# Kernel tuning notes

Hardware: AMD Instinct MI355X
Metric: run time of the kernel (lower is better)

The kernel has to match this reference:

```python
import jax, jax.numpy as jnp
import numpy as np

B, S, D, H, DK, DL, DR = 2, 2048, 2048, 16, 128, 512, 64
EPS = 1e-6


def _rmsnorm(x, w):
    # torch nn.RMSNorm: x / sqrt(mean(x^2) + eps) * weight, over last dim
    return x * jax.lax.rsqrt(jnp.mean(x * x, axis=-1, keepdims=True) + EPS) * w


def _rope_tables(seq_len, d):
    # matches RoPE.__init__: half of the d//2 freqs are real, half are zero
    quarter = d // 4
    freq = (1.0 / 10000.0) ** jnp.linspace(0.0, 1.0, quarter, dtype=jnp.float32)
    freq = jnp.concatenate([freq, jnp.zeros((quarter,), jnp.float32)])
    theta = jnp.arange(seq_len, dtype=jnp.float32)[:, None] * freq[None, :]  # (S, d//2)
    return jnp.cos(theta), jnp.sin(theta)


def _apply_rope(x, cos, sin):
    # x: (B, H, S, d); cos/sin: (S, d//2)
    half = x.shape[-1] // 2
    x1, x2 = x[..., :half], x[..., half:]
    c = cos[None, None, :, :]
    s = sin[None, None, :, :]
    y1 = x1 * c + x2 * s
    y2 = -x1 * s + x2 * c
    return jnp.concatenate([y1, y2], axis=-1)


def setup_inputs() -> dict:
    key = jax.random.key(0)
    ks = jax.random.split(key, 9)
    w = lambda k, sh: jax.random.normal(k, sh, jnp.float32) * 0.02
    return {
        "x": jax.random.normal(ks[0], (B, S, D), jnp.float32),
        "wq": w(ks[1], (D, H * DK)),
        "w_kv_down": w(ks[2], (D, DL)),
        "w_k_rope": w(ks[3], (DL, H * DR)),
        "w_k_nope": w(ks[4], (DL, H * (DK - DR))),
        "wv": w(ks[5], (DL, H * DK)),
        "wo": w(ks[6], (H * DK, D)),
        "q_norm_w": jnp.ones((DK,), jnp.float32),
        "k_norm_w": jnp.ones((DK,), jnp.float32),
    }


def reference(x, wq, w_kv_down, w_k_rope, w_k_nope, wv, wo, q_norm_w, k_norm_w):
    b, s, _ = x.shape
    # Q path
    q = (x @ wq).reshape(b, s, H, DK)
    q = _rmsnorm(q, q_norm_w).transpose(0, 2, 1, 3)  # (B,H,S,DK)
    # low-rank KV latent
    latent = x @ w_kv_down  # (B,S,DL)
    v = (latent @ wv).reshape(b, s, H, DK).transpose(0, 2, 1, 3)
    k_rope = (latent @ w_k_rope).reshape(b, s, H, DR).transpose(0, 2, 1, 3)
    k_nope = (latent @ w_k_nope).reshape(b, s, H, DK - DR).transpose(0, 2, 1, 3)
    # decoupled RoPE on first DR dims of q and on k_rope
    cos, sin = _rope_tables(s, DR)
    q = jnp.concatenate([_apply_rope(q[..., :DR], cos, sin), q[..., DR:]], axis=-1)
    k = jnp.concatenate([_apply_rope(k_rope, cos, sin), k_nope], axis=-1)
    k = _rmsnorm(k, k_norm_w)
    # causal SDPA, scale 1/sqrt(DK)
    scale = 1.0 / np.sqrt(DK).astype(np.float32)
    scores = jnp.einsum('bhqd,bhkd->bhqk', q, k) * scale
    causal = jnp.tril(jnp.ones((s, s), bool))
    scores = jnp.where(causal[None, None], scores, jnp.finfo(scores.dtype).min)
    attn = jax.nn.softmax(scores, axis=-1)
    out = jnp.einsum('bhqk,bhkd->bhqd', attn, v)
    out = out.transpose(0, 2, 1, 3).reshape(b, s, H * DK)
    return out @ wo
```

## Files before the change

### kernel.cpp

```cpp
#include <hip/hip_runtime.h>
#include <hip/hip_bf16.h>
#include <math.h>

#define B_ 2
#define S_ 2048
#define D_ 2048
#define H_ 16
#define DK_ 128
#define DL_ 512
#define DR_ 64
#define BS_ (B_ * S_)

typedef __attribute__((ext_vector_type(8))) short short8;
typedef __attribute__((ext_vector_type(4))) float f32x4;

static __device__ __forceinline__ ushort f2b(float f) {
    union { __hip_bfloat16 h; ushort u; } cvt;
    cvt.h = __float2bfloat16(f);
    return cvt.u;
}
static __device__ __forceinline__ float b2f(ushort u) {
    return __uint_as_float(((uint)u) << 16);
}

#define GLOAD_LDS16(g, l)                                                         \
    __builtin_amdgcn_global_load_lds(                                             \
        (const __attribute__((address_space(1))) void*)(g),                       \
        (__attribute__((address_space(3))) void*)(l), 16, 0, 0)

__global__ __launch_bounds__(256) void cvt_f32_bf16(const float* __restrict__ in,
                                                    ushort* __restrict__ out, int n) {
    int i = (blockIdx.x * 256 + threadIdx.x) * 4;
    if (i >= n) return;
    float4 v = *(const float4*)(in + i);
    ushort4 o;
    o.x = f2b(v.x); o.y = f2b(v.y); o.z = f2b(v.z); o.w = f2b(v.w);
    *(ushort4*)(out + i) = o;
}

__global__ __launch_bounds__(256) void transpose_cvt(const float* __restrict__ in,
                                                     ushort* __restrict__ out,
                                                     int R, int C) {
    __shared__ float tile[32][33];
    int c0 = blockIdx.x * 32, r0 = blockIdx.y * 32;
    int tx = threadIdx.x, ty = threadIdx.y;
#pragma unroll
    for (int i = 0; i < 4; ++i)
        tile[ty + i * 8][tx] = in[(size_t)(r0 + ty + i * 8) * C + c0 + tx];
    __syncthreads();
#pragma unroll
    for (int i = 0; i < 4; ++i)
        out[(size_t)(c0 + ty + i * 8) * R + r0 + tx] = f2b(tile[tx][ty + i * 8]);
}

__global__ __launch_bounds__(256) void v_transpose(const ushort* __restrict__ krnv,
                                                   ushort* __restrict__ vt) {
    __shared__ ushort tile[32][34];
    const int bh = blockIdx.z, b = bh >> 4, h = bh & 15;
    const int d0 = blockIdx.x * 32, s0 = blockIdx.y * 32;
    const int tx = threadIdx.x, ty = threadIdx.y;
    const ushort* src = krnv + (size_t)(b * 2048 + s0) * 4096 + 2048 + h * 128 + d0;
#pragma unroll
    for (int i = 0; i < 4; ++i)
        tile[ty + i * 8][tx] = src[(size_t)(ty + i * 8) * 4096 + tx];
    __syncthreads();
    ushort* dst = vt + ((size_t)bh * 128 + d0) * 2048 + s0;
#pragma unroll
    for (int i = 0; i < 4; ++i)
        dst[(size_t)(ty + i * 8) * 2048 + tx] = tile[tx][ty + i * 8];
}

__global__ __launch_bounds__(256) void rope_tables(float* __restrict__ cosT,
                                                   float* __restrict__ sinT) {
    int idx = blockIdx.x * 256 + threadIdx.x;
    int s = idx >> 5, j = idx & 31;
    float c = 1.f, sn = 0.f;
    if (j < 16) {
        float t = (float)j * (1.0f / 15.0f);
        float f = powf(10000.0f, -t);
        float th = (float)s * f;
        c = cosf(th);
        sn = sinf(th);
    }
    cosT[idx] = c;
    sinT[idx] = sn;
}

template <int OUT_BF16>
__global__ __launch_bounds__(256) void gemm_bt(const ushort* __restrict__ A,
                                               const ushort* __restrict__ BT,
                                               void* __restrict__ Cv,
                                               int M, int N, int K) {
    __shared__ __align__(16) ushort As[128 * 32];
    __shared__ __align__(16) ushort Bs[128 * 32];
    const int tid = threadIdx.x;
    const int lane = tid & 63, wave = tid >> 6;
    const int wr = wave >> 1, wc = wave & 1;
    const int row0 = blockIdx.y * 128, col0 = blockIdx.x * 128;
    const int fr = lane & 15, kg = (lane >> 4) * 8;

    f32x4 acc[4][4] = {};

    const int sr = tid >> 2;
    const int sc8 = (tid & 3) * 8;
    const ushort* ga = A + (size_t)(row0 + sr) * K + sc8;
    const ushort* gb = BT + (size_t)(col0 + sr) * K + sc8;
    ushort* asDst = As + (size_t)(wave * 64) * 8;
    ushort* bsDst = Bs + (size_t)(wave * 64) * 8;

    for (int k0 = 0; k0 < K; k0 += 32) {
        GLOAD_LDS16(ga + k0, asDst);
        GLOAD_LDS16(ga + (size_t)64 * K + k0, asDst + 256 * 8);
        GLOAD_LDS16(gb + k0, bsDst);
        GLOAD_LDS16(gb + (size_t)64 * K + k0, bsDst + 256 * 8);
        __syncthreads();

        short8 af[4], bfr[4];
#pragma unroll
        for (int m = 0; m < 4; ++m)
            af[m] = *(const short8*)&As[(wr * 64 + m * 16 + fr) * 32 + kg];
#pragma unroll
        for (int n = 0; n < 4; ++n)
            bfr[n] = *(const short8*)&Bs[(wc * 64 + n * 16 + fr) * 32 + kg];
#pragma unroll
        for (int m = 0; m < 4; ++m)
#pragma unroll
            for (int n = 0; n < 4; ++n)
                acc[m][n] = __builtin_amdgcn_mfma_f32_16x16x32_bf16(af[m], bfr[n],
                                                                    acc[m][n], 0, 0, 0);
        __syncthreads();
    }

    const int rbase = row0 + wr * 64 + (lane >> 4) * 4;
    const int cbase = col0 + wc * 64 + fr;
    if constexpr (OUT_BF16) {
        ushort* C = (ushort*)Cv;
#pragma unroll
        for (int m = 0; m < 4; ++m)
#pragma unroll
            for (int n = 0; n < 4; ++n)
#pragma unroll
                for (int j = 0; j < 4; ++j)
                    C[(size_t)(rbase + m * 16 + j) * N + cbase + n * 16] = f2b(acc[m][n][j]);
    } else {
        float* C = (float*)Cv;
#pragma unroll
        for (int m = 0; m < 4; ++m)
#pragma unroll
            for (int n = 0; n < 4; ++n)
#pragma unroll
                for (int j = 0; j < 4; ++j)
                    C[(size_t)(rbase + m * 16 + j) * N + cbase + n * 16] = acc[m][n][j];
    }
}

__global__ __launch_bounds__(256) void q_norm_rope(const ushort* __restrict__ qp,
                                                   const float* __restrict__ w,
                                                   const float* __restrict__ cosT,
                                                   const float* __restrict__ sinT,
                                                   ushort* __restrict__ qb) {
    const int lane = threadIdx.x & 63, wave = threadIdx.x >> 6;
    const int rowId = blockIdx.x * 4 + wave;
    const int bs = rowId >> 4, h = rowId & 15;
    const int s = bs & (S_ - 1);
    const float scale = 0.08838834764831845f;
    const ushort* src = qp + (size_t)bs * 2048 + h * 128;
    float e0 = b2f(src[lane]), e1 = b2f(src[64 + lane]);
    float ss = e0 * e0 + e1 * e1;
#pragma unroll
    for (int m = 1; m < 64; m <<= 1) ss += __shfl_xor(ss, m, 64);
    float r = rsqrtf(ss * (1.0f / 128.0f) + 1e-6f);
    float xn0 = e0 * r * w[lane];
    float xn1 = e1 * r * w[64 + lane];
    int j = lane & 31;
    float c = cosT[s * 32 + j], sn = sinT[s * 32 + j];
    float p = __shfl_xor(xn0, 32, 64);
    float y0 = (lane < 32) ? (xn0 * c + p * sn) : (-p * sn + xn0 * c);
    ushort* dst = qb + (size_t)bs * 2048 + h * 128;
    dst[lane] = f2b(y0 * scale);
    dst[64 + lane] = f2b(xn1 * scale);
}

__global__ __launch_bounds__(256) void k_assemble(const ushort* __restrict__ krnv,
                                                  const float* __restrict__ w,
                                                  const float* __restrict__ cosT,
                                                  const float* __restrict__ sinT,
                                                  ushort* __restrict__ kb) {
    const int lane = threadIdx.x & 63, wave = threadIdx.x >> 6;
    const int rowId = blockIdx.x * 4 + wave;
    const int bs = rowId >> 4, h = rowId & 15;
    const int s = bs & (S_ - 1);
    float e0 = b2f(krnv[(size_t)bs * 4096 + h * 64 + lane]);
    float e1 = b2f(krnv[(size_t)bs * 4096 + 1024 + h * 64 + lane]);
    int j = lane & 31;
    float c = cosT[s * 32 + j], sn = sinT[s * 32 + j];
    float p = __shfl_xor(e0, 32, 64);
    float y0 = (lane < 32) ? (e0 * c + p * sn) : (-p * sn + e0 * c);
    float ss = y0 * y0 + e1 * e1;
#pragma unroll
    for (int m = 1; m < 64; m <<= 1) ss += __shfl_xor(ss, m, 64);
    float r = rsqrtf(ss * (1.0f / 128.0f) + 1e-6f);
    ushort* dst = kb + (size_t)bs * 2048 + h * 128;
    dst[lane] = f2b(y0 * r * w[lane]);
    dst[64 + lane] = f2b(e1 * r * w[64 + lane]);
}

__global__ __launch_bounds__(512) void attn_fwd(const ushort* __restrict__ Q,
                                                const ushort* __restrict__ Kb,
                                                const ushort* __restrict__ Vt,
                                                ushort* __restrict__ Ob) {
    __shared__ __align__(16) ushort Kls[2][8192];
    __shared__ __align__(16) ushort Vls[2][8192];
    __shared__ __align__(16) ushort Pls[8][1024];
    const int tid = threadIdx.x, lane = tid & 63, wave = tid >> 6;
    const int bh = (int)blockIdx.x * 4 + ((int)blockIdx.y & 3);
    const int qp = (int)blockIdx.y >> 2;
    const int b = bh >> 4, h = bh & 15;
    const int fr = lane & 15, g = lane >> 4;
    const int sfr = lane >> 2, sg = lane & 3;

    const ushort* qbase = Q + (size_t)(b * S_) * 2048 + h * 128;
    const ushort* kbase = Kb + (size_t)(b * S_) * 2048 + h * 128;
    const ushort* vtbase = Vt + (size_t)bh * 128 * 2048;
    ushort* myP = Pls[wave];

    auto stage = [&](int kt0, int bufi) {
#pragma unroll
        for (int i = 0; i < 2; ++i) {
            const int si = wave * 2 + i;
            GLOAD_LDS16(kbase + (size_t)(kt0 + (si >> 2) * 16 + sfr) * 2048 +
                            (si & 3) * 32 + sg * 8,
                        &Kls[bufi][si * 512]);
            GLOAD_LDS16(vtbase + (size_t)((si >> 1) * 16 + sfr) * 2048 + kt0 +
                            (si & 1) * 32 + sg * 8,
                        &Vls[bufi][si * 512]);
        }
    };

#pragma unroll 1
    for (int pi = 0; pi < 2; ++pi) {
        const int qi = pi ? qp : 15 - qp;
        const int q0 = qi * 128;
        const int nt = 2 * qi + 2;

        short8 qf[4];
        const ushort* qrow = qbase + (size_t)(q0 + wave * 16 + fr) * 2048;
#pragma unroll
        for (int kb = 0; kb < 4; ++kb) qf[kb] = *(const short8*)(qrow + kb * 32 + g * 8);

        f32x4 Oacc[8] = {};
        float mrow[4], lrow[4];
#pragma unroll
        for (int j = 0; j < 4; ++j) { mrow[j] = -1e30f; lrow[j] = 0.f; }

        stage(0, 0);
        for (int t = 0; t < nt; ++t) {
            __syncthreads();
            if (t + 1 < nt) stage((t + 1) * 64, (t + 1) & 1);
            const ushort* Kc = Kls[t & 1];
            const ushort* Vc = Vls[t & 1];
            const int kt0 = t * 64;
            f32x4 sc[4] = {};
            __builtin_amdgcn_s_setprio(1);
#pragma unroll
            for (int n = 0; n < 4; ++n)
#pragma unroll
                for (int kb = 0; kb < 4; ++kb) {
                    short8 kf = *(const short8*)&Kc[(n * 4 + kb) * 512 + fr * 32 + g * 8];
                    sc[n] = __builtin_amdgcn_mfma_f32_16x16x32_bf16(qf[kb], kf, sc[n], 0, 0, 0);
                }
            __builtin_amdgcn_s_setprio(0);
            if (t >= nt - 2) {
#pragma unroll
                for (int n = 0; n < 4; ++n) {
                    int kpos = kt0 + n * 16 + fr;
#pragma unroll
                    for (int j = 0; j < 4; ++j) {
                        int qr = q0 + wave * 16 + g * 4 + j;
                        if (kpos > qr) sc[n][j] = -1e30f;
                    }
                }
            }
            float tmax[4];
#pragma unroll
            for (int j = 0; j < 4; ++j)
                tmax[j] = fmaxf(fmaxf(sc[0][j], sc[1][j]), fmaxf(sc[2][j], sc[3][j]));
#pragma unroll
            for (int m = 1; m < 16; m <<= 1)
#pragma unroll
                for (int j = 0; j < 4; ++j) tmax[j] = fmaxf(tmax[j], __shfl_xor(tmax[j], m, 64));
            float dm = fmaxf(fmaxf(tmax[0] - mrow[0], tmax[1] - mrow[1]),
                             fmaxf(tmax[2] - mrow[2], tmax[3] - mrow[3]));
            if (!__all(dm <= 8.0f)) {
                float alpha[4];
#pragma unroll
                for (int j = 0; j < 4; ++j) {
                    float mn = fmaxf(mrow[j], tmax[j]);
                    alpha[j] = __expf(mrow[j] - mn);
                    mrow[j] = mn;
                    lrow[j] *= alpha[j];
                }
#pragma unroll
                for (int n8 = 0; n8 < 8; ++n8)
#pragma unroll
                    for (int j = 0; j < 4; ++j) Oacc[n8][j] *= alpha[j];
            }
            float rsum[4] = {0.f, 0.f, 0.f, 0.f};
#pragma unroll
            for (int n = 0; n < 4; ++n)
#pragma unroll
                for (int j = 0; j < 4; ++j) {
                    float pv = __expf(sc[n][j] - mrow[j]);
                    sc[n][j] = pv;
                    rsum[j] += pv;
                }
#pragma unroll
            for (int m = 1; m < 16; m <<= 1)
#pragma unroll
                for (int j = 0; j < 4; ++j) rsum[j] += __shfl_xor(rsum[j], m, 64);
#pragma unroll
            for (int j = 0; j < 4; ++j) lrow[j] += rsum[j];
#pragma unroll
            for (int n = 0; n < 4; ++n)
#pragma unroll
                for (int j = 0; j < 4; ++j) {
                    int q = g * 4 + j;
                    int cg = n * 2 + (fr >> 3);
                    int cs = (((cg ^ (q >> 1)) & 7) << 3) | (fr & 7);
                    myP[q * 64 + cs] = f2b(sc[n][j]);
                }
            short8 pa[2];
#pragma unroll
            for (int ks = 0; ks < 2; ++ks) {
                int pg = ((ks * 4 + g) ^ (fr >> 1)) & 7;
                pa[ks] = *(const short8*)&myP[fr * 64 + (pg << 3)];
            }
            __builtin_amdgcn_s_setprio(1);
#pragma unroll
            for (int n8 = 0; n8 < 8; ++n8)
#pragma unroll
                for (int ks = 0; ks < 2; ++ks) {
                    short8 vf = *(const short8*)&Vc[(n8 * 2 + ks) * 512 + fr * 32 + g * 8];
                    Oacc[n8] = __builtin_amdgcn_mfma_f32_16x16x32_bf16(pa[ks], vf, Oacc[n8], 0, 0, 0);
                }
            __builtin_amdgcn_s_setprio(0);
        }
#pragma unroll
        for (int j = 0; j < 4; ++j) {
            int qr = q0 + wave * 16 + g * 4 + j;
            float inv = 1.0f / lrow[j];
            ushort* orow = Ob + (size_t)(b * S_ + qr) * 2048 + h * 128;
#pragma unroll
            for (int n8 = 0; n8 < 8; ++n8) orow[n8 * 16 + fr] = f2b(Oacc[n8][j] * inv);
        }
        __syncthreads();
    }
}

extern "C" void kernel_launch(void* const* d_in, const int* in_sizes, int n_in,
                              void* d_out, int out_size, void* d_ws, size_t ws_size,
                              hipStream_t stream) {
    (void)in_sizes; (void)n_in; (void)out_size; (void)ws_size;
    const float* x = (const float*)d_in[0];
    const float* wq = (const float*)d_in[1];
    const float* w_kv_down = (const float*)d_in[2];
    const float* w_k_rope = (const float*)d_in[3];
    const float* w_k_nope = (const float*)d_in[4];
    const float* wv = (const float*)d_in[5];
    const float* wo = (const float*)d_in[6];
    const float* q_norm_w = (const float*)d_in[7];
    const float* k_norm_w = (const float*)d_in[8];
    float* out = (float*)d_out;

    char* ws = (char*)d_ws;
    size_t off = 0;
    auto alloc = [&](size_t bytes) {
        off = (off + 255) & ~(size_t)255;
        void* p = ws + off;
        off += bytes;
        return p;
    };
    ushort* xb = (ushort*)alloc((size_t)BS_ * 2048 * 2);
    ushort* wq_t = (ushort*)alloc((size_t)2048 * 2048 * 2);
    ushort* wkv_t = (ushort*)alloc((size_t)512 * 2048 * 2);
    ushort* wkrnv_t = (ushort*)alloc((size_t)4096 * 512 * 2);
    ushort* wo_t = (ushort*)alloc((size_t)2048 * 2048 * 2);
    ushort* q_pre_b = (ushort*)alloc((size_t)BS_ * 2048 * 2);
    ushort* latent_b = (ushort*)alloc((size_t)BS_ * 512 * 2);
    ushort* krnv_b = (ushort*)alloc((size_t)BS_ * 4096 * 2);
    ushort* q_b = (ushort*)alloc((size_t)BS_ * 2048 * 2);
    ushort* k_b = (ushort*)alloc((size_t)BS_ * 2048 * 2);
    ushort* vt = (ushort*)alloc((size_t)BS_ * 2048 * 2);
    ushort* ao_b = (ushort*)alloc((size_t)BS_ * 2048 * 2);
    float* cosT = (float*)alloc((size_t)S_ * 32 * 4);
    float* sinT = (float*)alloc((size_t)S_ * 32 * 4);

    cvt_f32_bf16<<<(BS_ * 2048 / 4 + 255) / 256, 256, 0, stream>>>(x, xb, BS_ * 2048);
    transpose_cvt<<<dim3(2048 / 32, 2048 / 32), dim3(32, 8), 0, stream>>>(wq, wq_t, 2048, 2048);
    transpose_cvt<<<dim3(512 / 32, 2048 / 32), dim3(32, 8), 0, stream>>>(w_kv_down, wkv_t, 2048, 512);
    transpose_cvt<<<dim3(1024 / 32, 512 / 32), dim3(32, 8), 0, stream>>>(w_k_rope, wkrnv_t, 512, 1024);
    transpose_cvt<<<dim3(1024 / 32, 512 / 32), dim3(32, 8), 0, stream>>>(w_k_nope, wkrnv_t + (size_t)1024 * 512, 512, 1024);
    transpose_cvt<<<dim3(2048 / 32, 512 / 32), dim3(32, 8), 0, stream>>>(wv, wkrnv_t + (size_t)2048 * 512, 512, 2048);
    transpose_cvt<<<dim3(2048 / 32, 2048 / 32), dim3(32, 8), 0, stream>>>(wo, wo_t, 2048, 2048);
    rope_tables<<<S_ * 32 / 256, 256, 0, stream>>>(cosT, sinT);

    gemm_bt<1><<<dim3(2048 / 128, BS_ / 128), 256, 0, stream>>>(xb, wq_t, q_pre_b, BS_, 2048, 2048);
    gemm_bt<1><<<dim3(512 / 128, BS_ / 128), 256, 0, stream>>>(xb, wkv_t, latent_b, BS_, 512, 2048);
    gemm_bt<1><<<dim3(4096 / 128, BS_ / 128), 256, 0, stream>>>(latent_b, wkrnv_t, krnv_b, BS_, 4096, 512);

    q_norm_rope<<<BS_ * H_ / 4, 256, 0, stream>>>(q_pre_b, q_norm_w, cosT, sinT, q_b);
    k_assemble<<<BS_ * H_ / 4, 256, 0, stream>>>(krnv_b, k_norm_w, cosT, sinT, k_b);

    v_transpose<<<dim3(128 / 32, 2048 / 32, B_ * H_), dim3(32, 8), 0, stream>>>(krnv_b, vt);

    attn_fwd<<<dim3(8, B_ * H_), 512, 0, stream>>>(q_b, k_b, vt, ao_b);

    gemm_bt<0><<<dim3(2048 / 128, BS_ / 128), 256, 0, stream>>>(ao_b, wo_t, out, BS_, 2048, 2048);
}
```

Before: 455.3 us.

## Merge prep, projection and epilogue launches; split attention into one q-tile per block

Folds the conversion, transpose and RoPE-table kernels into one prep launch, and fuses the Q and latent GEMMs into one grid. Q norm/RoPE, K assembly and the V transpose also become one epilogue launch. The aim is to cut launch overhead and tail idle time between small kernels. The attention kernel no longer processes a paired short and long q-tile per block. It now launches 512 blocks, one q-tile each, longest first, which trades causal load balancing for more parallelism.

Result: faster. 395.8 us (-13.1%).

```diff
diff --git a/kernel.cpp b/kernel.cpp
--- a/kernel.cpp
+++ b/kernel.cpp
@@ -28,22 +28,12 @@
         (const __attribute__((address_space(1))) void*)(g),                       \
         (__attribute__((address_space(3))) void*)(l), 16, 0, 0)
 
-__global__ __launch_bounds__(256) void cvt_f32_bf16(const float* __restrict__ in,
-                                                    ushort* __restrict__ out, int n) {
-    int i = (blockIdx.x * 256 + threadIdx.x) * 4;
-    if (i >= n) return;
-    float4 v = *(const float4*)(in + i);
-    ushort4 o;
-    o.x = f2b(v.x); o.y = f2b(v.y); o.z = f2b(v.z); o.w = f2b(v.w);
-    *(ushort4*)(out + i) = o;
-}
-
-__global__ __launch_bounds__(256) void transpose_cvt(const float* __restrict__ in,
-                                                     ushort* __restrict__ out,
-                                                     int R, int C) {
-    __shared__ float tile[32][33];
-    int c0 = blockIdx.x * 32, r0 = blockIdx.y * 32;
-    int tx = threadIdx.x, ty = threadIdx.y;
+static __device__ __forceinline__ void tr_cvt(const float* __restrict__ in,
+                                              ushort* __restrict__ out,
+                                              int R, int C, int bx, int by,
+                                              float (*tile)[33]) {
+    const int tx = threadIdx.x & 31, ty = threadIdx.x >> 5;
+    const int c0 = bx * 32, r0 = by * 32;
 #pragma unroll
     for (int i = 0; i < 4; ++i)
         tile[ty + i * 8][tx] = in[(size_t)(r0 + ty + i * 8) * C + c0 + tx];
@@ -53,50 +43,71 @@
         out[(size_t)(c0 + ty + i * 8) * R + r0 + tx] = f2b(tile[tx][ty + i * 8]);
 }
 
-__global__ __launch_bounds__(256) void v_transpose(const ushort* __restrict__ krnv,
-                                                   ushort* __restrict__ vt) {
-    __shared__ ushort tile[32][34];
-    const int bh = blockIdx.z, b = bh >> 4, h = bh & 15;
-    const int d0 = blockIdx.x * 32, s0 = blockIdx.y * 32;
-    const int tx = threadIdx.x, ty = threadIdx.y;
-    const ushort* src = krnv + (size_t)(b * 2048 + s0) * 4096 + 2048 + h * 128 + d0;
-#pragma unroll
-    for (int i = 0; i < 4; ++i)
-        tile[ty + i * 8][tx] = src[(size_t)(ty + i * 8) * 4096 + tx];
-    __syncthreads();
-    ushort* dst = vt + ((size_t)bh * 128 + d0) * 2048 + s0;
-#pragma unroll
-    for (int i = 0; i < 4; ++i)
-        dst[(size_t)(ty + i * 8) * 2048 + tx] = tile[tx][ty + i * 8];
-}
-
-__global__ __launch_bounds__(256) void rope_tables(float* __restrict__ cosT,
-                                                   float* __restrict__ sinT) {
-    int idx = blockIdx.x * 256 + threadIdx.x;
-    int s = idx >> 5, j = idx & 31;
-    float c = 1.f, sn = 0.f;
-    if (j < 16) {
-        float t = (float)j * (1.0f / 15.0f);
-        float f = powf(10000.0f, -t);
-        float th = (float)s * f;
-        c = cosf(th);
-        sn = sinf(th);
-    }
-    cosT[idx] = c;
-    sinT[idx] = sn;
+__global__ __launch_bounds__(256) void prep(const float* __restrict__ x,
+                                            ushort* __restrict__ xb,
+                                            const float* __restrict__ wq,
+                                            ushort* __restrict__ wq_t,
+                                            const float* __restrict__ wkv,
+                                            ushort* __restrict__ wkv_t,
+                                            const float* __restrict__ wkr,
+                                            const float* __restrict__ wkn,
+                                            const float* __restrict__ wv,
+                                            ushort* __restrict__ wkrnv_t,
+                                            const float* __restrict__ wo,
+                                            ushort* __restrict__ wo_t,
+                                            float* __restrict__ cosT,
+                                            float* __restrict__ sinT) {
+    __shared__ float tile[32][33];
+    const int id = blockIdx.x, tid = threadIdx.x;
+    if (id < 8192) {
+        int i = (id * 256 + tid) * 4;
+        float4 v = *(const float4*)(x + i);
+        ushort4 o;
+        o.x = f2b(v.x); o.y = f2b(v.y); o.z = f2b(v.z); o.w = f2b(v.w);
+        *(ushort4*)(xb + i) = o;
+    } else if (id < 12288) {
+        int l = id - 8192;
+        tr_cvt(wq, wq_t, 2048, 2048, l & 63, l >> 6, tile);
+    } else if (id < 13312) {
+        int l = id - 12288;
+        tr_cvt(wkv, wkv_t, 2048, 512, l & 15, l >> 4, tile);
+    } else if (id < 13824) {
+        int l = id - 13312;
+        tr_cvt(wkr, wkrnv_t, 512, 1024, l & 31, l >> 5, tile);
+    } else if (id < 14336) {
+        int l = id - 13824;
+        tr_cvt(wkn, wkrnv_t + (size_t)1024 * 512, 512, 1024, l & 31, l >> 5, tile);
+    } else if (id < 15360) {
+        int l = id - 14336;
+        tr_cvt(wv, wkrnv_t + (size_t)2048 * 512, 512, 2048, l & 63, l >> 6, tile);
+    } else if (id < 19456) {
+        int l = id - 15360;
+        tr_cvt(wo, wo_t, 2048, 2048, l & 63, l >> 6, tile);
+    } else {
+        int idx = (id - 19456) * 256 + tid;
+        int s = idx >> 5, j = idx & 31;
+        float c = 1.f, sn = 0.f;
+        if (j < 16) {
+            float t = (float)j * (1.0f / 15.0f);
+            float f = powf(10000.0f, -t);
+            float th = (float)s * f;
+            c = cosf(th);
+            sn = sinf(th);
+        }
+        cosT[idx] = c;
+        sinT[idx] = sn;
+    }
 }
 
 template <int OUT_BF16>
-__global__ __launch_bounds__(256) void gemm_bt(const ushort* __restrict__ A,
-                                               const ushort* __restrict__ BT,
-                                               void* __restrict__ Cv,
-                                               int M, int N, int K) {
-    __shared__ __align__(16) ushort As[128 * 32];
-    __shared__ __align__(16) ushort Bs[128 * 32];
+static __device__ __forceinline__ void gemm_body(const ushort* __restrict__ A,
+                                                 const ushort* __restrict__ BT,
+                                                 void* __restrict__ Cv,
+                                                 int N, int K, int row0, int col0,
+                                                 ushort* As, ushort* Bs) {
     const int tid = threadIdx.x;
     const int lane = tid & 63, wave = tid >> 6;
     const int wr = wave >> 1, wc = wave & 1;
-    const int row0 = blockIdx.y * 128, col0 = blockIdx.x * 128;
     const int fr = lane & 15, kg = (lane >> 4) * 8;
 
     f32x4 acc[4][4] = {};
@@ -154,55 +165,95 @@
     }
 }
 
-__global__ __launch_bounds__(256) void q_norm_rope(const ushort* __restrict__ qp,
-                                                   const float* __restrict__ w,
-                                                   const float* __restrict__ cosT,
-                                                   const float* __restrict__ sinT,
-                                                   ushort* __restrict__ qb) {
+template <int OUT_BF16>
+__global__ __launch_bounds__(256) void gemm_bt(const ushort* __restrict__ A,
+                                               const ushort* __restrict__ BT,
+                                               void* __restrict__ Cv,
+                                               int N, int K) {
+    __shared__ __align__(16) ushort As[128 * 32];
+    __shared__ __align__(16) ushort Bs[128 * 32];
+    gemm_body<OUT_BF16>(A, BT, Cv, N, K, blockIdx.y * 128, blockIdx.x * 128, As, Bs);
+}
+
+__global__ __launch_bounds__(256) void gemm_qlat(const ushort* __restrict__ A,
+                                                 const ushort* __restrict__ wq_t,
+                                                 const ushort* __restrict__ wkv_t,
+                                                 ushort* __restrict__ qp,
+                                                 ushort* __restrict__ lat) {
+    __shared__ __align__(16) ushort As[128 * 32];
+    __shared__ __align__(16) ushort Bs[128 * 32];
+    const int bx = blockIdx.x;
+    if (bx < 16)
+        gemm_body<1>(A, wq_t, qp, 2048, 2048, blockIdx.y * 128, bx * 128, As, Bs);
+    else
+        gemm_body<1>(A, wkv_t, lat, 512, 2048, blockIdx.y * 128, (bx - 16) * 128, As, Bs);
+}
+
+__global__ __launch_bounds__(256) void epi(const ushort* __restrict__ qp,
+                                           const ushort* __restrict__ krnv,
+                                           const float* __restrict__ qw,
+                                           const float* __restrict__ kw,
+                                           const float* __restrict__ cosT,
+                                           const float* __restrict__ sinT,
+                                           ushort* __restrict__ qb,
+                                           ushort* __restrict__ kb,
+                                           ushort* __restrict__ vt) {
+    __shared__ ushort tile[32][34];
+    const int id = blockIdx.x;
     const int lane = threadIdx.x & 63, wave = threadIdx.x >> 6;
-    const int rowId = blockIdx.x * 4 + wave;
-    const int bs = rowId >> 4, h = rowId & 15;
-    const int s = bs & (S_ - 1);
-    const float scale = 0.08838834764831845f;
-    const ushort* src = qp + (size_t)bs * 2048 + h * 128;
-    float e0 = b2f(src[lane]), e1 = b2f(src[64 + lane]);
-    float ss = e0 * e0 + e1 * e1;
-#pragma unroll
-    for (int m = 1; m < 64; m <<= 1) ss += __shfl_xor(ss, m, 64);
-    float r = rsqrtf(ss * (1.0f / 128.0f) + 1e-6f);
-    float xn0 = e0 * r * w[lane];
-    float xn1 = e1 * r * w[64 + lane];
-    int j = lane & 31;
-    float c = cosT[s * 32 + j], sn = sinT[s * 32 + j];
-    float p = __shfl_xor(xn0, 32, 64);
-    float y0 = (lane < 32) ? (xn0 * c + p * sn) : (-p * sn + xn0 * c);
-    ushort* dst = qb + (size_t)bs * 2048 + h * 128;
-    dst[lane] = f2b(y0 * scale);
-    dst[64 + lane] = f2b(xn1 * scale);
-}
-
-__global__ __launch_bounds__(256) void k_assemble(const ushort* __restrict__ krnv,
-                                                  const float* __restrict__ w,
-                                                  const float* __restrict__ cosT,
-                                                  const float* __restrict__ sinT,
-                                                  ushort* __restrict__ kb) {
-    const int lane = threadIdx.x & 63, wave = threadIdx.x >> 6;
-    const int rowId = blockIdx.x * 4 + wave;
-    const int bs = rowId >> 4, h = rowId & 15;
-    const int s = bs & (S_ - 1);
-    float e0 = b2f(krnv[(size_t)bs * 4096 + h * 64 + lane]);
-    float e1 = b2f(krnv[(size_t)bs * 4096 + 1024 + h * 64 + lane]);
-    int j = lane & 31;
-    float c = cosT[s * 32 + j], sn = sinT[s * 32 + j];
-    float p = __shfl_xor(e0, 32, 64);
-    float y0 = (lane < 32) ? (e0 * c + p * sn) : (-p * sn + e0 * c);
-    float ss = y0 * y0 + e1 * e1;
-#pragma unroll
-    for (int m = 1; m < 64; m <<= 1) ss += __shfl_xor(ss, m, 64);
-    float r = rsqrtf(ss * (1.0f / 128.0f) + 1e-6f);
-    ushort* dst = kb + (size_t)bs * 2048 + h * 128;
-    dst[lane] = f2b(y0 * r * w[lane]);
-    dst[64 + lane] = f2b(e1 * r * w[64 + lane]);
+    if (id < 16384) {
+        const int rowId = id * 4 + wave;
+        const int bs = rowId >> 4, h = rowId & 15;
+        const int s = bs & (S_ - 1);
+        const float scale = 0.08838834764831845f;
+        const ushort* src = qp + (size_t)bs * 2048 + h * 128;
+        float e0 = b2f(src[lane]), e1 = b2f(src[64 + lane]);
+        float ss = e0 * e0 + e1 * e1;
+#pragma unroll
+        for (int m = 1; m < 64; m <<= 1) ss += __shfl_xor(ss, m, 64);
+        float r = rsqrtf(ss * (1.0f / 128.0f) + 1e-6f);
+        float xn0 = e0 * r * qw[lane];
+        float xn1 = e1 * r * qw[64 + lane];
+        int j = lane & 31;
+        float c = cosT[s * 32 + j], sn = sinT[s * 32 + j];
+        float p = __shfl_xor(xn0, 32, 64);
+        float y0 = (lane < 32) ? (xn0 * c + p * sn) : (-p * sn + xn0 * c);
+        ushort* dst = qb + (size_t)bs * 2048 + h * 128;
+        dst[lane] = f2b(y0 * scale);
+        dst[64 + lane] = f2b(xn1 * scale);
+    } else if (id < 32768) {
+        const int rowId = (id - 16384) * 4 + wave;
+        const int bs = rowId >> 4, h = rowId & 15;
+        const int s = bs & (S_ - 1);
+        float e0 = b2f(krnv[(size_t)bs * 4096 + h * 64 + lane]);
+        float e1 = b2f(krnv[(size_t)bs * 4096 + 1024 + h * 64 + lane]);
+        int j = lane & 31;
+        float c = cosT[s * 32 + j], sn = sinT[s * 32 + j];
+        float p = __shfl_xor(e0, 32, 64);
+        float y0 = (lane < 32) ? (e0 * c + p * sn) : (-p * sn + e0 * c);
+        float ss = y0 * y0 + e1 * e1;
+#pragma unroll
+        for (int m = 1; m < 64; m <<= 1) ss += __shfl_xor(ss, m, 64);
+        float r = rsqrtf(ss * (1.0f / 128.0f) + 1e-6f);
+        ushort* dst = kb + (size_t)bs * 2048 + h * 128;
+        dst[lane] = f2b(y0 * r * kw[lane]);
+        dst[64 + lane] = f2b(e1 * r * kw[64 + lane]);
+    } else {
+        const int l = id - 32768;
+        const int bx = l & 3, by = (l >> 2) & 63, bh = l >> 8;
+        const int b = bh >> 4, h = bh & 15;
+        const int d0 = bx * 32, s0 = by * 32;
+        const int tx = threadIdx.x & 31, ty = threadIdx.x >> 5;
+        const ushort* src = krnv + (size_t)(b * 2048 + s0) * 4096 + 2048 + h * 128 + d0;
+#pragma unroll
+        for (int i = 0; i < 4; ++i)
+            tile[ty + i * 8][tx] = src[(size_t)(ty + i * 8) * 4096 + tx];
+        __syncthreads();
+        ushort* dst = vt + ((size_t)bh * 128 + d0) * 2048 + s0;
+#pragma unroll
+        for (int i = 0; i < 4; ++i)
+            dst[(size_t)(ty + i * 8) * 2048 + tx] = tile[tx][ty + i * 8];
+    }
 }
 
 __global__ __launch_bounds__(512) void attn_fwd(const ushort* __restrict__ Q,
@@ -213,8 +264,9 @@
     __shared__ __align__(16) ushort Vls[2][8192];
     __shared__ __align__(16) ushort Pls[8][1024];
     const int tid = threadIdx.x, lane = tid & 63, wave = tid >> 6;
-    const int bh = (int)blockIdx.x * 4 + ((int)blockIdx.y & 3);
-    const int qp = (int)blockIdx.y >> 2;
+    const int bhx = blockIdx.x;
+    const int bh = (bhx & 7) * 4 + (bhx >> 3);
+    const int qi = 15 - (int)blockIdx.y;
     const int b = bh >> 4, h = bh & 15;
     const int fr = lane & 15, g = lane >> 4;
     const int sfr = lane >> 2, sg = lane & 3;
@@ -237,123 +289,118 @@
         }
     };
 
-#pragma unroll 1
-    for (int pi = 0; pi < 2; ++pi) {
-        const int qi = pi ? qp : 15 - qp;
-        const int q0 = qi * 128;
-        const int nt = 2 * qi + 2;
-
-        short8 qf[4];
-        const ushort* qrow = qbase + (size_t)(q0 + wave * 16 + fr) * 2048;
-#pragma unroll
-        for (int kb = 0; kb < 4; ++kb) qf[kb] = *(const short8*)(qrow + kb * 32 + g * 8);
-
-        f32x4 Oacc[8] = {};
-        float mrow[4], lrow[4];
-#pragma unroll
-        for (int j = 0; j < 4; ++j) { mrow[j] = -1e30f; lrow[j] = 0.f; }
-
-        stage(0, 0);
-        for (int t = 0; t < nt; ++t) {
-            __syncthreads();
-            if (t + 1 < nt) stage((t + 1) * 64, (t + 1) & 1);
-            const ushort* Kc = Kls[t & 1];
-            const ushort* Vc = Vls[t & 1];
-            const int kt0 = t * 64;
-            f32x4 sc[4] = {};
-            __builtin_amdgcn_s_setprio(1);
-#pragma unroll
-            for (int n = 0; n < 4; ++n)
-#pragma unroll
-                for (int kb = 0; kb < 4; ++kb) {
-                    short8 kf = *(const short8*)&Kc[(n * 4 + kb) * 512 + fr * 32 + g * 8];
-                    sc[n] = __builtin_amdgcn_mfma_f32_16x16x32_bf16(qf[kb], kf, sc[n], 0, 0, 0);
+    const int q0 = qi * 128;
+    const int nt = 2 * qi + 2;
+
+    short8 qf[4];
+    const ushort* qrow = qbase + (size_t)(q0 + wave * 16 + fr) * 2048;
+#pragma unroll
+    for (int kb = 0; kb < 4; ++kb) qf[kb] = *(const short8*)(qrow + kb * 32 + g * 8);
+
+    f32x4 Oacc[8] = {};
+    float mrow[4], lrow[4];
+#pragma unroll
+    for (int j = 0; j < 4; ++j) { mrow[j] = -1e30f; lrow[j] = 0.f; }
+
+    stage(0, 0);
+    for (int t = 0; t < nt; ++t) {
+        __syncthreads();
+        if (t + 1 < nt) stage((t + 1) * 64, (t + 1) & 1);
+        const ushort* Kc = Kls[t & 1];
+        const ushort* Vc = Vls[t & 1];
+        const int kt0 = t * 64;
+        f32x4 sc[4] = {};
+        __builtin_amdgcn_s_setprio(1);
+#pragma unroll
+        for (int n = 0; n < 4; ++n)
+#pragma unroll
+            for (int kb = 0; kb < 4; ++kb) {
+                short8 kf = *(const short8*)&Kc[(n * 4 + kb) * 512 + fr * 32 + g * 8];
+                sc[n] = __builtin_amdgcn_mfma_f32_16x16x32_bf16(qf[kb], kf, sc[n], 0, 0, 0);
+            }
+        __builtin_amdgcn_s_setprio(0);
+        if (t >= nt - 2) {
+#pragma unroll
+            for (int n = 0; n < 4; ++n) {
+                int kpos = kt0 + n * 16 + fr;
+#pragma unroll
+                for (int j = 0; j < 4; ++j) {
+                    int qr = q0 + wave * 16 + g * 4 + j;
+                    if (kpos > qr) sc[n][j] = -1e30f;
                 }
-            __builtin_amdgcn_s_setprio(0);
-            if (t >= nt - 2) {
-#pragma unroll
-                for (int n = 0; n < 4; ++n) {
-                    int kpos = kt0 + n * 16 + fr;
-#pragma unroll
-                    for (int j = 0; j < 4; ++j) {
-                        int qr = q0 + wave * 16 + g * 4 + j;
-                        if (kpos > qr) sc[n][j] = -1e30f;
-                    }
-                }
-            }
-            float tmax[4];
-#pragma unroll
-            for (int j = 0; j < 4; ++j)
-                tmax[j] = fmaxf(fmaxf(sc[0][j], sc[1][j]), fmaxf(sc[2][j], sc[3][j]));
-#pragma unroll
-            for (int m = 1; m < 16; m <<= 1)
-#pragma unroll
-                for (int j = 0; j < 4; ++j) tmax[j] = fmaxf(tmax[j], __shfl_xor(tmax[j], m, 64));
-            float dm = fmaxf(fmaxf(tmax[0] - mrow[0], tmax[1] - mrow[1]),
-                             fmaxf(tmax[2] - mrow[2], tmax[3] - mrow[3]));
-            if (!__all(dm <= 8.0f)) {
-                float alpha[4];
-#pragma unroll
-                for (int j = 0; j < 4; ++j) {
-                    float mn = fmaxf(mrow[j], tmax[j]);
-                    alpha[j] = __expf(mrow[j] - mn);
-                    mrow[j] = mn;
-                    lrow[j] *= alpha[j];
-                }
-#pragma unroll
-                for (int n8 = 0; n8 < 8; ++n8)
-#pragma unroll
-                    for (int j = 0; j < 4; ++j) Oacc[n8][j] *= alpha[j];
-            }
-            float rsum[4] = {0.f, 0.f, 0.f, 0.f};
-#pragma unroll
-            for (int n = 0; n < 4; ++n)
-#pragma unroll
-                for (int j = 0; j < 4; ++j) {
-                    float pv = __expf(sc[n][j] - mrow[j]);
-                    sc[n][j] = pv;
-                    rsum[j] += pv;
-                }
-#pragma unroll
-            for (int m = 1; m < 16; m <<= 1)
-#pragma unroll
-                for (int j = 0; j < 4; ++j) rsum[j] += __shfl_xor(rsum[j], m, 64);
-#pragma unroll
-            for (int j = 0; j < 4; ++j) lrow[j] += rsum[j];
-#pragma unroll
-            for (int n = 0; n < 4; ++n)
-#pragma unroll
-                for (int j = 0; j < 4; ++j) {
-                    int q = g * 4 + j;
-                    int cg = n * 2 + (fr >> 3);
-                    int cs = (((cg ^ (q >> 1)) & 7) << 3) | (fr & 7);
-                    myP[q * 64 + cs] = f2b(sc[n][j]);
-                }
-            short8 pa[2];
+            }
+        }
+        float tmax[4];
+#pragma unroll
+        for (int j = 0; j < 4; ++j)
+            tmax[j] = fmaxf(fmaxf(sc[0][j], sc[1][j]), fmaxf(sc[2][j], sc[3][j]));
+#pragma unroll
+        for (int m = 1; m < 16; m <<= 1)
+#pragma unroll
+            for (int j = 0; j < 4; ++j) tmax[j] = fmaxf(tmax[j], __shfl_xor(tmax[j], m, 64));
+        float dm = fmaxf(fmaxf(tmax[0] - mrow[0], tmax[1] - mrow[1]),
+                         fmaxf(tmax[2] - mrow[2], tmax[3] - mrow[3]));
+        if (!__all(dm <= 8.0f)) {
+            float alpha[4];
+#pragma unroll
+            for (int j = 0; j < 4; ++j) {
+                float mn = fmaxf(mrow[j], tmax[j]);
+                alpha[j] = __expf(mrow[j] - mn);
+                mrow[j] = mn;
+                lrow[j] *= alpha[j];
+            }
+#pragma unroll
+            for (int n8 = 0; n8 < 8; ++n8)
+#pragma unroll
+                for (int j = 0; j < 4; ++j) Oacc[n8][j] *= alpha[j];
+        }
+        float rsum[4] = {0.f, 0.f, 0.f, 0.f};
+#pragma unroll
+        for (int n = 0; n < 4; ++n)
+#pragma unroll
+            for (int j = 0; j < 4; ++j) {
+                float pv = __expf(sc[n][j] - mrow[j]);
+                sc[n][j] = pv;
+                rsum[j] += pv;
+            }
+#pragma unroll
+        for (int m = 1; m < 16; m <<= 1)
+#pragma unroll
+            for (int j = 0; j < 4; ++j) rsum[j] += __shfl_xor(rsum[j], m, 64);
+#pragma unroll
+        for (int j = 0; j < 4; ++j) lrow[j] += rsum[j];
+#pragma unroll
+        for (int n = 0; n < 4; ++n)
+#pragma unroll
+            for (int j = 0; j < 4; ++j) {
+                int q = g * 4 + j;
+                int cg = n * 2 + (fr >> 3);
+                int cs = (((cg ^ (q >> 1)) & 7) << 3) | (fr & 7);
+                myP[q * 64 + cs] = f2b(sc[n][j]);
+            }
+        short8 pa[2];
+#pragma unroll
+        for (int ks = 0; ks < 2; ++ks) {
+            int pg = ((ks * 4 + g) ^ (fr >> 1)) & 7;
+            pa[ks] = *(const short8*)&myP[fr * 64 + (pg << 3)];
+        }
+        __builtin_amdgcn_s_setprio(1);
+#pragma unroll
+        for (int n8 = 0; n8 < 8; ++n8)
 #pragma unroll
             for (int ks = 0; ks < 2; ++ks) {
-                int pg = ((ks * 4 + g) ^ (fr >> 1)) & 7;
-                pa[ks] = *(const short8*)&myP[fr * 64 + (pg << 3)];
-            }
-            __builtin_amdgcn_s_setprio(1);
-#pragma unroll
-            for (int n8 = 0; n8 < 8; ++n8)
-#pragma unroll
-                for (int ks = 0; ks < 2; ++ks) {
-                    short8 vf = *(const short8*)&Vc[(n8 * 2 + ks) * 512 + fr * 32 + g * 8];
-                    Oacc[n8] = __builtin_amdgcn_mfma_f32_16x16x32_bf16(pa[ks], vf, Oacc[n8], 0, 0, 0);
-                }
-            __builtin_amdgcn_s_setprio(0);
-        }
-#pragma unroll
-        for (int j = 0; j < 4; ++j) {
-            int qr = q0 + wave * 16 + g * 4 + j;
-            float inv = 1.0f / lrow[j];
-            ushort* orow = Ob + (size_t)(b * S_ + qr) * 2048 + h * 128;
-#pragma unroll
-            for (int n8 = 0; n8 < 8; ++n8) orow[n8 * 16 + fr] = f2b(Oacc[n8][j] * inv);
-        }
-        __syncthreads();
+                short8 vf = *(const short8*)&Vc[(n8 * 2 + ks) * 512 + fr * 32 + g * 8];
+                Oacc[n8] = __builtin_amdgcn_mfma_f32_16x16x32_bf16(pa[ks], vf, Oacc[n8], 0, 0, 0);
+            }
+        __builtin_amdgcn_s_setprio(0);
+    }
+#pragma unroll
+    for (int j = 0; j < 4; ++j) {
+        int qr = q0 + wave * 16 + g * 4 + j;
+        float inv = 1.0f / lrow[j];
+        ushort* orow = Ob + (size_t)(b * S_ + qr) * 2048 + h * 128;
+#pragma unroll
+        for (int n8 = 0; n8 < 8; ++n8) orow[n8 * 16 + fr] = f2b(Oacc[n8][j] * inv);
     }
 }
 
@@ -395,25 +442,13 @@
     float* cosT = (float*)alloc((size_t)S_ * 32 * 4);
     float* sinT = (float*)alloc((size_t)S_ * 32 * 4);
 
-    cvt_f32_bf16<<<(BS_ * 2048 / 4 + 255) / 256, 256, 0, stream>>>(x, xb, BS_ * 2048);
-    transpose_cvt<<<dim3(2048 / 32, 2048 / 32), dim3(32, 8), 0, stream>>>(wq, wq_t, 2048, 2048);
-    transpose_cvt<<<dim3(512 / 32, 2048 / 32), dim3(32, 8), 0, stream>>>(w_kv_down, wkv_t, 2048, 512);
-    transpose_cvt<<<dim3(1024 / 32, 512 / 32), dim3(32, 8), 0, stream>>>(w_k_rope, wkrnv_t, 512, 1024);
-    transpose_cvt<<<dim3(1024 / 32, 512 / 32), dim3(32, 8), 0, stream>>>(w_k_nope, wkrnv_t + (size_t)1024 * 512, 512, 1024);
-    transpose_cvt<<<dim3(2048 / 32, 512 / 32), dim3(32, 8), 0, stream>>>(wv, wkrnv_t + (size_t)2048 * 512, 512, 2048);
-    transpose_cvt<<<dim3(2048 / 32, 2048 / 32), dim3(32, 8), 0, stream>>>(wo, wo_t, 2048, 2048);
-    rope_tables<<<S_ * 32 / 256, 256, 0, stream>>>(cosT, sinT);
-
-    gemm_bt<1><<<dim3(2048 / 128, BS_ / 128), 256, 0, stream>>>(xb, wq_t, q_pre_b, BS_, 2048, 2048);
-    gemm_bt<1><<<dim3(512 / 128, BS_ / 128), 256, 0, stream>>>(xb, wkv_t, latent_b, BS_, 512, 2048);
-    gemm_bt<1><<<dim3(4096 / 128, BS_ / 128), 256, 0, stream>>>(latent_b, wkrnv_t, krnv_b, BS_, 4096, 512);
-
-    q_norm_rope<<<BS_ * H_ / 4, 256, 0, stream>>>(q_pre_b, q_norm_w, cosT, sinT, q_b);
-    k_assemble<<<BS_ * H_ / 4, 256, 0, stream>>>(krnv_b, k_norm_w, cosT, sinT, k_b);
-
-    v_transpose<<<dim3(128 / 32, 2048 / 32, B_ * H_), dim3(32, 8), 0, stream>>>(krnv_b, vt);
-
-    attn_fwd<<<dim3(8, B_ * H_), 512, 0, stream>>>(q_b, k_b, vt, ao_b);
-
-    gemm_bt<0><<<dim3(2048 / 128, BS_ / 128), 256, 0, stream>>>(ao_b, wo_t, out, BS_, 2048, 2048);
-}
+    prep<<<19712, 256, 0, stream>>>(x, xb, wq, wq_t, w_kv_down, wkv_t,
+                                    w_k_rope, w_k_nope, wv, wkrnv_t, wo, wo_t,
+                                    cosT, sinT);
+    gemm_qlat<<<dim3(20, 32), 256, 0, stream>>>(xb, wq_t, wkv_t, q_pre_b, latent_b);
+    gemm_bt<1><<<dim3(32, 32), 256, 0, stream>>>(latent_b, wkrnv_t, krnv_b, 4096, 512);
+    epi<<<40960, 256, 0, stream>>>(q_pre_b, krnv_b, q_norm_w, k_norm_w,
+                                   cosT, sinT, q_b, k_b, vt);
+    attn_fwd<<<dim3(32, 16), 512, 0, stream>>>(q_b, k_b, vt, ao_b);
+    gemm_bt<0><<<dim3(16, 32), 256, 0, stream>>>(ao_b, wo_t, out, 2048, 2048);
+}
```
